# Performance work log

Hardware: AMD Instinct MI355X
Metric: run time of the kernel (lower is better)

The kernel has to match this reference:

```python
import jax, jax.numpy as jnp
import numpy as np

N_HEAD = 32
N_QUERY_GROUPS = 8
HEAD_SIZE = 128
N_EMBD = 4096


def apply_rope(x, cos, sin):
    # x: [B, H, T, D]; cos/sin: [T, D] (rotary_percentage = 1.0 so D = head_size)
    d = x.shape[-1]
    x1, x2 = x[..., : d // 2], x[..., d // 2:]
    rotated = jnp.concatenate([-x2, x1], axis=-1)
    return x * cos + rotated * sin


def setup_inputs() -> dict:
    key = jax.random.key(0)
    k1, k2, k3, k4, k5 = jax.random.split(key, 5)
    B, T = 1, 2048
    x = jax.random.normal(k1, (B, T, N_EMBD), dtype=jnp.float32)
    # realistic rope angles
    theta = 10000.0 ** (-jnp.arange(0, HEAD_SIZE // 2, dtype=jnp.float32) * 2.0 / HEAD_SIZE)
    ang = jnp.arange(T, dtype=jnp.float32)[:, None] * theta[None, :]
    ang = jnp.concatenate([ang, ang], axis=-1)  # [T, HEAD_SIZE]
    cos, sin = jnp.cos(ang), jnp.sin(ang)
    qkv_dim = (N_HEAD + 2 * N_QUERY_GROUPS) * HEAD_SIZE  # 6144
    w_attn = jax.random.normal(k2, (qkv_dim, N_EMBD), dtype=jnp.float32) * (N_EMBD ** -0.5)
    w_proj = jax.random.normal(k3, (N_EMBD, N_HEAD * HEAD_SIZE), dtype=jnp.float32) * ((N_HEAD * HEAD_SIZE) ** -0.5)
    return {"x": x, "cos": cos, "sin": sin, "w_attn": w_attn, "w_proj": w_proj}


def reference(x, cos, sin, w_attn, w_proj):
    B, T, C = x.shape
    G, hs = N_QUERY_GROUPS, HEAD_SIZE
    q_per_kv = N_HEAD // G  # 4
    total_qkv = q_per_kv + 2

    qkv = jnp.einsum('btc,oc->bto', x, w_attn)  # [B, T, 6144]
    qkv = qkv.reshape(B, T, G, total_qkv, hs).transpose(0, 2, 3, 1, 4)  # [B, G, total, T, hs]
    q = qkv[:, :, :q_per_kv]              # [B, G, qpk, T, hs]
    k = qkv[:, :, q_per_kv:q_per_kv + 1]  # [B, G, 1,   T, hs]
    v = qkv[:, :, q_per_kv + 1:]          # [B, G, 1,   T, hs]

    # GQA expand to per-query heads, then flatten head dims
    k = jnp.broadcast_to(k, (B, G, q_per_kv, T, hs))
    v = jnp.broadcast_to(v, (B, G, q_per_kv, T, hs))
    q = q.reshape(B, N_HEAD, T, hs)
    k = k.reshape(B, N_HEAD, T, hs)
    v = v.reshape(B, N_HEAD, T, hs)

    # rotary_percentage = 1.0 -> rope over full head dim
    q = apply_rope(q, cos, sin)
    k = apply_rope(k, cos, sin)

    scale = 1.0 / jnp.sqrt(jnp.float32(hs))
    scores = jnp.einsum('bhqd,bhkd->bhqk', q, k) * scale  # [B, H, T, T]
    causal = jnp.tril(jnp.ones((T, T), dtype=bool))
    scores = jnp.where(causal, scores, jnp.finfo(scores.dtype).min)
    attn = jax.nn.softmax(scores, axis=-1)
    y = jnp.einsum('bhqk,bhkd->bhqd', attn, v)  # [B, H, T, hs]
    y = y.transpose(0, 2, 1, 3).reshape(B, T, N_HEAD * hs)
    return jnp.einsum('bto,co->btc', y, w_proj)  # [B, T, C]
```

## Files before the change

kernel.cpp:

```cpp
#include <hip/hip_runtime.h>
#include <hip/hip_bf16.h>

typedef __attribute__((ext_vector_type(8))) short short8;
typedef __attribute__((ext_vector_type(4))) float f32x4;

__device__ inline unsigned short f2bf(float f) {
  __hip_bfloat16 h = __float2bfloat16(f);
  return *reinterpret_cast<unsigned short*>(&h);
}
__device__ inline float bf2f(unsigned short u) {
  union { unsigned u; float f; } v; v.u = ((unsigned)u) << 16;
  return v.f;
}

#define GLOAD_LDS16(g, l)                                          \
  __builtin_amdgcn_global_load_lds(                                \
      (const __attribute__((address_space(1))) void*)(g),          \
      (__attribute__((address_space(3))) void*)(l), 16, 0, 0)

__global__ void f32_to_bf16(const float* __restrict__ in,
                            unsigned short* __restrict__ out, int n8) {
  int i = blockIdx.x * 256 + threadIdx.x;
  if (i >= n8) return;
  const float4* p = (const float4*)in + (size_t)i * 2;
  float4 a = p[0], b = p[1];
  short8 v;
  v[0] = f2bf(a.x); v[1] = f2bf(a.y); v[2] = f2bf(a.z); v[3] = f2bf(a.w);
  v[4] = f2bf(b.x); v[5] = f2bf(b.y); v[6] = f2bf(b.z); v[7] = f2bf(b.w);
  *((short8*)out + i) = v;
}

template <bool OUT_F32>
__global__ __launch_bounds__(256, 3)
void gemm_bt_bf16(const unsigned short* __restrict__ A,
                  const unsigned short* __restrict__ B,
                  void* __restrict__ Cp, int M, int N, int K) {
  __shared__ __align__(16) unsigned short As[128 * 32];
  __shared__ __align__(16) unsigned short Bs[128 * 32];
  const int t = threadIdx.x;
  const int lane = t & 63, w = t >> 6;
  const int wr = w >> 1, wc = w & 1;
  const int r16 = lane & 15, kg = lane >> 4;
  const int bm = blockIdx.x, bn = blockIdx.y;

  const int srow = w * 16 + (lane >> 2);
  const int scol = (lane & 3) * 8;

  const unsigned short* Ag = A + (size_t)(bm * 128) * K;
  const unsigned short* Bg = B + (size_t)(bn * 128) * K;

  f32x4 acc[4][4] = {};

  for (int k0 = 0; k0 < K; k0 += 32) {
    __syncthreads();
#pragma unroll
    for (int i = 0; i < 2; ++i) {
      GLOAD_LDS16(Ag + (size_t)(i * 64 + srow) * K + k0 + scol,
                  As + i * 2048 + w * 512);
      GLOAD_LDS16(Bg + (size_t)(i * 64 + srow) * K + k0 + scol,
                  Bs + i * 2048 + w * 512);
    }
    __syncthreads();

    short8 a[4], b[4];
#pragma unroll
    for (int m = 0; m < 4; ++m)
      a[m] = *(const short8*)&As[(wr * 64 + m * 16 + r16) * 32 + kg * 8];
#pragma unroll
    for (int n = 0; n < 4; ++n)
      b[n] = *(const short8*)&Bs[(wc * 64 + n * 16 + r16) * 32 + kg * 8];
#pragma unroll
    for (int m = 0; m < 4; ++m)
#pragma unroll
      for (int n = 0; n < 4; ++n)
        acc[m][n] = __builtin_amdgcn_mfma_f32_16x16x32_bf16(a[m], b[n], acc[m][n], 0, 0, 0);
  }

#pragma unroll
  for (int m = 0; m < 4; ++m) {
#pragma unroll
    for (int n = 0; n < 4; ++n) {
#pragma unroll
      for (int j = 0; j < 4; ++j) {
        int row = bm * 128 + wr * 64 + m * 16 + kg * 4 + j;
        int col = bn * 128 + wc * 64 + n * 16 + r16;
        if (OUT_F32) ((float*)Cp)[(size_t)row * N + col] = acc[m][n][j];
        else ((unsigned short*)Cp)[(size_t)row * N + col] = f2bf(acc[m][n][j]);
      }
    }
  }
}

__global__ void rope_qk(const unsigned short* __restrict__ qkv,
                        const float* __restrict__ cosb, const float* __restrict__ sinb,
                        unsigned short* __restrict__ Q, unsigned short* __restrict__ K) {
  int pair = blockIdx.x * 4 + (threadIdx.x >> 6);
  int l = threadIdx.x & 63;
  int t = pair / 40, slot = pair - t * 40;
  const unsigned short* src;
  unsigned short* dst;
  float scale;
  if (slot < 32) {
    int g = slot >> 2, j = slot & 3;
    src = qkv + (size_t)t * 6144 + g * 768 + j * 128;
    dst = Q + ((size_t)slot * 2048 + t) * 128;
    scale = 0.08838834764831845f;
  } else {
    int g = slot - 32;
    src = qkv + (size_t)t * 6144 + g * 768 + 512;
    dst = K + ((size_t)g * 2048 + t) * 128;
    scale = 1.0f;
  }
  float x1 = bf2f(src[l]), x2 = bf2f(src[64 + l]);
  float c1 = cosb[t * 128 + l], s1 = sinb[t * 128 + l];
  float c2 = cosb[t * 128 + 64 + l], s2 = sinb[t * 128 + 64 + l];
  dst[l]      = f2bf((x1 * c1 - x2 * s1) * scale);
  dst[64 + l] = f2bf((x2 * c2 + x1 * s2) * scale);
}

__global__ void transpose_v(const unsigned short* __restrict__ qkv,
                            unsigned short* __restrict__ Vt) {
  __shared__ __align__(16) unsigned short tile[64][136];
  int g = blockIdx.y, t0 = blockIdx.x * 64;
  int th = threadIdx.x;
  int r = th >> 2, c0 = (th & 3) * 32;
  const unsigned short* src = qkv + (size_t)(t0 + r) * 6144 + g * 768 + 640 + c0;
#pragma unroll
  for (int i = 0; i < 4; ++i)
    *(short8*)&tile[r][c0 + i * 8] = *(const short8*)(src + i * 8);
  __syncthreads();
  int d = th >> 1, tc = (th & 1) * 32;
  unsigned short* dst = Vt + (size_t)(g * 128 + d) * 2048 + t0 + tc;
#pragma unroll
  for (int j = 0; j < 32; ++j) dst[j] = tile[tc + j][d];
}

__global__ __launch_bounds__(256, 2)
void flash_attn(const unsigned short* __restrict__ Q, const unsigned short* __restrict__ K,
                const unsigned short* __restrict__ Vt, unsigned short* __restrict__ Y) {
  __shared__ __align__(16) unsigned short Ksm[2][64 * 128];
  __shared__ __align__(16) unsigned short Vsm[2][128 * 64];

  const int h = blockIdx.y, g = h >> 2;
  const int t = threadIdx.x, lane = t & 63, w = t >> 6;
  const int r16 = lane & 15, kg = lane >> 4;
  const bool odd = kg & 1;
  const bool hi = kg >> 1;
  const bool useswap = odd ^ hi;

  const unsigned short* Kg = K + (size_t)g * 2048 * 128;
  const unsigned short* Vg = Vt + (size_t)g * 128 * 2048;

  const int krl = lane >> 4, kc = lane & 15;
  const int vrl = lane >> 3, vc = lane & 7;

  auto stage = [&](int kvs, int b) {
#pragma unroll
    for (int i = 0; i < 4; ++i) {
      int row = w * 16 + i * 4 + krl;
      int sc = kc ^ (row & 7);
      GLOAD_LDS16(Kg + (size_t)(kvs + row) * 128 + sc * 8,
                  &Ksm[b][(w * 16 + i * 4) * 128]);
    }
#pragma unroll
    for (int i = 0; i < 4; ++i) {
      int d = w * 32 + i * 8 + vrl;
      int sc = vc ^ (d & 7);
      GLOAD_LDS16(Vg + (size_t)d * 2048 + kvs + sc * 8,
                  &Vsm[b][(w * 32 + i * 8) * 64]);
    }
  };

  auto process = [&](int q0) {
    short8 qf[4];
    const unsigned short* qrow = Q + ((size_t)h * 2048 + q0 + w * 16 + r16) * 128;
#pragma unroll
    for (int kk = 0; kk < 4; ++kk) qf[kk] = *(const short8*)(qrow + kk * 32 + kg * 8);

    f32x4 o[8] = {};
    float mrow = -1e30f, lrow = 0.f;
    const int qg = q0 + w * 16 + r16;
    const int nt = q0 / 64 + 1;

    __syncthreads();
    stage(0, 0);

    for (int kt = 0; kt < nt; ++kt) {
      const int b = kt & 1;
      const int kv0 = kt * 64;
      __syncthreads();
      if (kt + 1 < nt) stage((kt + 1) * 64, b ^ 1);

      f32x4 s[4] = {};
      __builtin_amdgcn_s_setprio(1);
#pragma unroll
      for (int n = 0; n < 4; ++n) {
        int kr = n * 16 + r16;
#pragma unroll
        for (int kk = 0; kk < 4; ++kk) {
          short8 kf = *(const short8*)__builtin_assume_aligned(
              &Ksm[b][kr * 128 + ((kk * 32 + kg * 8) ^ ((kr & 7) << 3))], 16);
          s[n] = __builtin_amdgcn_mfma_f32_16x16x32_bf16(kf, qf[kk], s[n], 0, 0, 0);
        }
      }
      __builtin_amdgcn_s_setprio(0);

      if (kv0 + 63 > q0 + w * 16) {
#pragma unroll
        for (int n = 0; n < 4; ++n)
#pragma unroll
          for (int j = 0; j < 4; ++j)
            if (kv0 + n * 16 + kg * 4 + j > qg) s[n][j] = -1e30f;
      }

      float rmax = -1e30f;
#pragma unroll
      for (int n = 0; n < 4; ++n)
#pragma unroll
        for (int j = 0; j < 4; ++j) rmax = fmaxf(rmax, s[n][j]);
      rmax = fmaxf(rmax, __shfl_xor(rmax, 16));
      rmax = fmaxf(rmax, __shfl_xor(rmax, 32));

      if (__builtin_amdgcn_ballot_w64(rmax > mrow)) {
        float mnew = fmaxf(mrow, rmax);
        float fac = __expf(mrow - mnew);
        mrow = mnew;
        lrow *= fac;
        float fj[4];
#pragma unroll
        for (int j = 0; j < 4; ++j) fj[j] = __shfl(fac, kg * 4 + j);
#pragma unroll
        for (int f = 0; f < 8; ++f)
#pragma unroll
          for (int j = 0; j < 4; ++j) o[f][j] *= fj[j];
      }

      float p[4][4];
      float rs = 0.f;
#pragma unroll
      for (int n = 0; n < 4; ++n)
#pragma unroll
        for (int j = 0; j < 4; ++j) {
          p[n][j] = __expf(s[n][j] - mrow);
          rs += p[n][j];
        }
      rs += __shfl_xor(rs, 16);
      rs += __shfl_xor(rs, 32);
      lrow += rs;

      unsigned bpk[4][2], xpk[4][2];
#pragma unroll
      for (int n = 0; n < 4; ++n)
#pragma unroll
        for (int i = 0; i < 2; ++i)
          bpk[n][i] = (unsigned)f2bf(p[n][2 * i]) | ((unsigned)f2bf(p[n][2 * i + 1]) << 16);
#pragma unroll
      for (int n = 0; n < 4; ++n)
#pragma unroll
        for (int i = 0; i < 2; ++i) xpk[n][i] = __shfl_xor(bpk[n][i], 16);

      unsigned pl[4][2], ph[4][2];
#pragma unroll
      for (int n = 0; n < 4; ++n)
#pragma unroll
        for (int i = 0; i < 2; ++i) {
          pl[n][i] = odd ? xpk[n][i] : bpk[n][i];
          ph[n][i] = odd ? bpk[n][i] : xpk[n][i];
        }

      short8 pa[2];
#pragma unroll
      for (int kk = 0; kk < 2; ++kk) {
        unsigned kp0 = hi ? pl[2 * kk + 1][0] : pl[2 * kk][0];
        unsigned kp1 = hi ? pl[2 * kk + 1][1] : pl[2 * kk][1];
        unsigned kp2 = hi ? ph[2 * kk + 1][0] : ph[2 * kk][0];
        unsigned kp3 = hi ? ph[2 * kk + 1][1] : ph[2 * kk][1];
        unsigned sd0 = hi ? pl[2 * kk][0] : pl[2 * kk + 1][0];
        unsigned sd1 = hi ? pl[2 * kk][1] : pl[2 * kk + 1][1];
        unsigned sd2 = hi ? ph[2 * kk][0] : ph[2 * kk + 1][0];
        unsigned sd3 = hi ? ph[2 * kk][1] : ph[2 * kk + 1][1];
        unsigned g0 = __shfl_xor(sd0, 32), g1 = __shfl_xor(sd1, 32);
        unsigned g2 = __shfl_xor(sd2, 32), g3 = __shfl_xor(sd3, 32);
        union { unsigned u[4]; short8 v; } pu;
        pu.u[0] = useswap ? g0 : kp0;
        pu.u[1] = useswap ? g1 : kp1;
        pu.u[2] = useswap ? g2 : kp2;
        pu.u[3] = useswap ? g3 : kp3;
        pa[kk] = pu.v;
      }

      __builtin_amdgcn_s_setprio(1);
#pragma unroll
      for (int kk = 0; kk < 2; ++kk) {
#pragma unroll
        for (int f = 0; f < 8; ++f) {
          int d = f * 16 + r16;
          short8 vf = *(const short8*)__builtin_assume_aligned(
              &Vsm[b][d * 64 + ((kk * 32 + kg * 8) ^ ((d & 7) << 3))], 16);
          o[f] = __builtin_amdgcn_mfma_f32_16x16x32_bf16(pa[kk], vf, o[f], 0, 0, 0);
        }
      }
      __builtin_amdgcn_s_setprio(0);
    }

    float inv = 1.f / lrow;
    float invj[4];
#pragma unroll
    for (int j = 0; j < 4; ++j) invj[j] = __shfl(inv, kg * 4 + j);
#pragma unroll
    for (int j = 0; j < 4; ++j) {
      int row = q0 + w * 16 + kg * 4 + j;
      unsigned short* yr = Y + (size_t)row * 4096 + h * 128;
#pragma unroll
      for (int f = 0; f < 8; ++f) yr[f * 16 + r16] = f2bf(o[f][j] * invj[j]);
    }
  };

  const int pr = blockIdx.x;
  process(pr * 64);
  process((31 - pr) * 64);
}

extern "C" void kernel_launch(void* const* d_in, const int* in_sizes, int n_in,
                              void* d_out, int out_size, void* d_ws, size_t ws_size,
                              hipStream_t stream) {
  const float* x      = (const float*)d_in[0];
  const float* cosb   = (const float*)d_in[1];
  const float* sinb   = (const float*)d_in[2];
  const float* w_attn = (const float*)d_in[3];
  const float* w_proj = (const float*)d_in[4];
  float* out = (float*)d_out;

  char* ws = (char*)d_ws;
  const size_t MB = 1024 * 1024;
  unsigned short* Xb  = (unsigned short*)(ws);
  unsigned short* Wa  = (unsigned short*)(ws + 16 * MB);
  unsigned short* Wp  = (unsigned short*)(ws);
  unsigned short* Qb  = (unsigned short*)(ws + 32 * MB);
  unsigned short* Kb  = (unsigned short*)(ws + 48 * MB);
  unsigned short* Vt  = (unsigned short*)(ws + 52 * MB);
  unsigned short* qkv = (unsigned short*)(ws + 64 * MB);
  unsigned short* Yb  = (unsigned short*)(ws + 64 * MB);

  f32_to_bf16<<<4096, 256, 0, stream>>>(x, Xb, 2048 * 4096 / 8);
  f32_to_bf16<<<12288, 256, 0, stream>>>(w_attn, Wa, 6144 * 4096 / 8);
  gemm_bt_bf16<false><<<dim3(16, 48), 256, 0, stream>>>(Xb, Wa, qkv, 2048, 6144, 4096);
  rope_qk<<<20480, 256, 0, stream>>>(qkv, cosb, sinb, Qb, Kb);
  transpose_v<<<dim3(32, 8), 256, 0, stream>>>(qkv, Vt);
  f32_to_bf16<<<8192, 256, 0, stream>>>(w_proj, Wp, 4096 * 4096 / 8);
  flash_attn<<<dim3(16, 32), 256, 0, stream>>>(Qb, Kb, Vt, Yb);
  gemm_bt_bf16<true><<<dim3(16, 32), 256, 0, stream>>>(Yb, Wp, out, 2048, 4096, 4096);
}
```

Measured before the change: 351.6 us.

## Replace GEMM with 256-row tiled, double-buffered, swizzled LDS pipeline

Replaces the 128x128, single-buffered bf16 GEMM with a 512-thread kernel using 256xBN tiles, a K-step of 64, double-buffered LDS with async global-to-LDS prefetch two steps ahead, XOR-swizzled LDS layout, and interleaved MFMA phases with priority hints. It targets the per-step sync stalls, low data reuse and LDS bank conflicts of the old GEMM, for both the QKV and output projections. In exchange it uses much more LDS and registers, launches fewer blocks (192 and 256), and relies on fragile hand-placed waitcnt and barriers.

```diff
diff --git a/kernel.cpp b/kernel.cpp
--- a/kernel.cpp
+++ b/kernel.cpp
@@ -30,60 +30,142 @@
   *((short8*)out + i) = v;
 }
 
-template <bool OUT_F32>
-__global__ __launch_bounds__(256, 3)
-void gemm_bt_bf16(const unsigned short* __restrict__ A,
-                  const unsigned short* __restrict__ B,
-                  void* __restrict__ Cp, int M, int N, int K) {
-  __shared__ __align__(16) unsigned short As[128 * 32];
-  __shared__ __align__(16) unsigned short Bs[128 * 32];
-  const int t = threadIdx.x;
-  const int lane = t & 63, w = t >> 6;
-  const int wr = w >> 1, wc = w & 1;
+template <int BN, bool OUT_F32>
+__global__ __launch_bounds__(512, 2)
+void gemm256(const unsigned short* __restrict__ A, const unsigned short* __restrict__ B,
+             void* __restrict__ Cp, int M, int N, int K, int nbm) {
+  constexpr int BPARTS = BN / 128;
+  constexpr int WN = BN / 4;
+  constexpr int NREP = WN / 16;
+  constexpr int NQ = NREP / 2;
+  constexpr int LPK = 4 + 2 * BPARTS;
+
+  __shared__ __align__(16) unsigned short lds[2][2 + BPARTS][128 * 64];
+
+  const int t = threadIdx.x, lane = t & 63, w = t >> 6;
+  const int wm = w >> 2, wn = w & 3;
   const int r16 = lane & 15, kg = lane >> 4;
-  const int bm = blockIdx.x, bn = blockIdx.y;
-
-  const int srow = w * 16 + (lane >> 2);
-  const int scol = (lane & 3) * 8;
-
-  const unsigned short* Ag = A + (size_t)(bm * 128) * K;
-  const unsigned short* Bg = B + (size_t)(bn * 128) * K;
-
-  f32x4 acc[4][4] = {};
-
-  for (int k0 = 0; k0 < K; k0 += 32) {
-    __syncthreads();
+  const int bid = blockIdx.x;
+  const int bm = bid % nbm, bn = bid / nbm;
+  const int NT = K >> 6;
+
+  const int sr = lane >> 3, sch = lane & 7;
+  const unsigned short* Ag = A + (size_t)(bm * 256) * K;
+  const unsigned short* Bg = B + (size_t)(bn * BN) * K;
+
+  auto stageA = [&](int kt, int h, int b) {
 #pragma unroll
     for (int i = 0; i < 2; ++i) {
-      GLOAD_LDS16(Ag + (size_t)(i * 64 + srow) * K + k0 + scol,
-                  As + i * 2048 + w * 512);
-      GLOAD_LDS16(Bg + (size_t)(i * 64 + srow) * K + k0 + scol,
-                  Bs + i * 2048 + w * 512);
-    }
-    __syncthreads();
-
-    short8 a[4], b[4];
-#pragma unroll
-    for (int m = 0; m < 4; ++m)
-      a[m] = *(const short8*)&As[(wr * 64 + m * 16 + r16) * 32 + kg * 8];
-#pragma unroll
-    for (int n = 0; n < 4; ++n)
-      b[n] = *(const short8*)&Bs[(wc * 64 + n * 16 + r16) * 32 + kg * 8];
-#pragma unroll
-    for (int m = 0; m < 4; ++m)
-#pragma unroll
-      for (int n = 0; n < 4; ++n)
-        acc[m][n] = __builtin_amdgcn_mfma_f32_16x16x32_bf16(a[m], b[n], acc[m][n], 0, 0, 0);
+      int rb = w * 16 + i * 8;
+      int rl = rb + sr;
+      int sc = sch ^ (rl & 7);
+      GLOAD_LDS16(Ag + (size_t)(h * 128 + rl) * K + kt * 64 + sc * 8,
+                  &lds[b][h][rb * 64]);
+    }
+  };
+  auto stageB = [&](int kt, int h, int b) {
+#pragma unroll
+    for (int i = 0; i < 2; ++i) {
+      int rb = w * 16 + i * 8;
+      int rl = rb + sr;
+      int sc = sch ^ (rl & 7);
+      GLOAD_LDS16(Bg + (size_t)(h * 128 + rl) * K + kt * 64 + sc * 8,
+                  &lds[b][2 + h][rb * 64]);
+    }
+  };
+
+  const int bpart = (wn * WN) >> 7;
+  const int brow0 = (wn * WN) & 127;
+
+  auto lda = [&](int b, int m, int kk) -> short8 {
+    int rp = m * 16 + r16;
+    int ch = (kk * 4 + kg) ^ (rp & 7);
+    return *(const short8*)__builtin_assume_aligned(&lds[b][wm][rp * 64 + ch * 8], 16);
+  };
+  auto ldb = [&](int b, int n, int kk) -> short8 {
+    int rp = brow0 + n * 16 + r16;
+    int ch = (kk * 4 + kg) ^ (rp & 7);
+    return *(const short8*)__builtin_assume_aligned(&lds[b][2 + bpart][rp * 64 + ch * 8], 16);
+  };
+
+  f32x4 acc[8][NREP] = {};
+  short8 a0[4][2], a1[4][2], bb[NREP][2];
+
+#define MFMA_Q(AARR, MB, NB)                                                   \
+  _Pragma("unroll") for (int m = 0; m < 4; ++m)                                \
+  _Pragma("unroll") for (int n = 0; n < NQ; ++n)                               \
+  _Pragma("unroll") for (int kk = 0; kk < 2; ++kk)                             \
+      acc[MB + m][NB + n] = __builtin_amdgcn_mfma_f32_16x16x32_bf16(           \
+          AARR[m][kk], bb[NB + n][kk], acc[MB + m][NB + n], 0, 0, 0);
+
+#define LGKM0_FENCE()                                       \
+  asm volatile("s_waitcnt lgkmcnt(0)" ::: "memory");        \
+  __builtin_amdgcn_sched_barrier(0);
+
+  stageB(0, 0, 0); if (BPARTS == 2) stageB(0, 1, 0);
+  stageA(0, 0, 0); stageA(0, 1, 0);
+  stageB(1, 0, 1); if (BPARTS == 2) stageB(1, 1, 1);
+  stageA(1, 0, 1); stageA(1, 1, 1);
+  asm volatile("s_waitcnt vmcnt(%0)" :: "n"(LPK) : "memory");
+  __builtin_amdgcn_s_barrier();
+
+  for (int kt = 0; kt < NT; ++kt) {
+    const int b = kt & 1;
+    const bool pf = (kt + 2) < NT;
+
+#pragma unroll
+    for (int m = 0; m < 4; ++m) { a0[m][0] = lda(b, m, 0); a0[m][1] = lda(b, m, 1); }
+#pragma unroll
+    for (int n = 0; n < NQ; ++n) { bb[n][0] = ldb(b, n, 0); bb[n][1] = ldb(b, n, 1); }
+    __builtin_amdgcn_s_barrier();
+    LGKM0_FENCE();
+    __builtin_amdgcn_s_setprio(1);
+    MFMA_Q(a0, 0, 0);
+    __builtin_amdgcn_s_setprio(0);
+    __builtin_amdgcn_s_barrier();
+
+#pragma unroll
+    for (int n = 0; n < NQ; ++n) { bb[NQ + n][0] = ldb(b, NQ + n, 0); bb[NQ + n][1] = ldb(b, NQ + n, 1); }
+    __builtin_amdgcn_s_barrier();
+    LGKM0_FENCE();
+    __builtin_amdgcn_s_setprio(1);
+    MFMA_Q(a0, 0, NQ);
+    __builtin_amdgcn_s_setprio(0);
+    __builtin_amdgcn_s_barrier();
+
+#pragma unroll
+    for (int m = 0; m < 4; ++m) { a1[m][0] = lda(b, 4 + m, 0); a1[m][1] = lda(b, 4 + m, 1); }
+    if (pf) { stageB(kt + 2, 0, b); if (BPARTS == 2) stageB(kt + 2, 1, b); }
+    __builtin_amdgcn_s_barrier();
+    LGKM0_FENCE();
+    __builtin_amdgcn_s_setprio(1);
+    MFMA_Q(a1, 4, NQ);
+    __builtin_amdgcn_s_setprio(0);
+    __builtin_amdgcn_s_barrier();
+
+    if (pf) { stageA(kt + 2, 0, b); stageA(kt + 2, 1, b); }
+    __builtin_amdgcn_s_barrier();
+    __builtin_amdgcn_s_setprio(1);
+    MFMA_Q(a1, 4, 0);
+    __builtin_amdgcn_s_setprio(0);
+    if (kt + 1 < NT) {
+      if (pf) asm volatile("s_waitcnt vmcnt(%0)" :: "n"(LPK) : "memory");
+      else    asm volatile("s_waitcnt vmcnt(0)" ::: "memory");
+      __builtin_amdgcn_sched_barrier(0);
+      __builtin_amdgcn_s_barrier();
+    }
   }
-
-#pragma unroll
-  for (int m = 0; m < 4; ++m) {
-#pragma unroll
-    for (int n = 0; n < 4; ++n) {
+#undef MFMA_Q
+#undef LGKM0_FENCE
+
+#pragma unroll
+  for (int m = 0; m < 8; ++m) {
+#pragma unroll
+    for (int n = 0; n < NREP; ++n) {
 #pragma unroll
       for (int j = 0; j < 4; ++j) {
-        int row = bm * 128 + wr * 64 + m * 16 + kg * 4 + j;
-        int col = bn * 128 + wc * 64 + n * 16 + r16;
+        int row = bm * 256 + wm * 128 + m * 16 + kg * 4 + j;
+        int col = bn * BN + wn * WN + n * 16 + r16;
         if (OUT_F32) ((float*)Cp)[(size_t)row * N + col] = acc[m][n][j];
         else ((unsigned short*)Cp)[(size_t)row * N + col] = f2bf(acc[m][n][j]);
       }
@@ -344,10 +426,10 @@
 
   f32_to_bf16<<<4096, 256, 0, stream>>>(x, Xb, 2048 * 4096 / 8);
   f32_to_bf16<<<12288, 256, 0, stream>>>(w_attn, Wa, 6144 * 4096 / 8);
-  gemm_bt_bf16<false><<<dim3(16, 48), 256, 0, stream>>>(Xb, Wa, qkv, 2048, 6144, 4096);
+  gemm256<256, false><<<192, 512, 0, stream>>>(Xb, Wa, qkv, 2048, 6144, 4096, 8);
   rope_qk<<<20480, 256, 0, stream>>>(qkv, cosb, sinb, Qb, Kb);
   transpose_v<<<dim3(32, 8), 256, 0, stream>>>(qkv, Vt);
   f32_to_bf16<<<8192, 256, 0, stream>>>(w_proj, Wp, 4096 * 4096 / 8);
   flash_attn<<<dim3(16, 32), 256, 0, stream>>>(Qb, Kb, Vt, Yb);
-  gemm_bt_bf16<true><<<dim3(16, 32), 256, 0, stream>>>(Yb, Wp, out, 2048, 4096, 4096);
-}
+  gemm256<128, true><<<256, 512, 0, stream>>>(Yb, Wp, out, 2048, 4096, 4096, 8);
+}
```

After: 341.2 us. -3.0%, faster.

## Replace generic GEMM with pipelined, swizzled, larger-tile QKV and projection GEMMs

Applied to the files above, without the earlier changes.

Replaces the simple single-buffered 128x128x32 GEMM with two specialised 512-thread kernels. They use 256x192 and 128x256 tiles, K-step 64, double-buffered LDS filled by direct global-to-LDS loads, and an XOR swizzle to avoid LDS bank conflicts. Prefetch of later k-tiles is interleaved with MFMA phases, using explicit vmcnt waits, barriers and setprio so that memory traffic overlaps compute. Each launch is 256 blocks, one wave of work on the 256 CUs. The cost is much more hand-scheduled code and larger LDS and register use per block.

```diff
diff --git a/kernel.cpp b/kernel.cpp
--- a/kernel.cpp
+++ b/kernel.cpp
@@ -17,6 +17,12 @@
   __builtin_amdgcn_global_load_lds(                                \
       (const __attribute__((address_space(1))) void*)(g),          \
       (__attribute__((address_space(3))) void*)(l), 16, 0, 0)
+
+#define MFMA16(a, b, c) __builtin_amdgcn_mfma_f32_16x16x32_bf16((a), (b), (c), 0, 0, 0)
+
+#define LGKM0()                                              \
+  asm volatile("s_waitcnt lgkmcnt(0)" ::: "memory");         \
+  __builtin_amdgcn_sched_barrier(0);
 
 __global__ void f32_to_bf16(const float* __restrict__ in,
                             unsigned short* __restrict__ out, int n8) {
@@ -30,65 +36,215 @@
   *((short8*)out + i) = v;
 }
 
-template <bool OUT_F32>
-__global__ __launch_bounds__(256, 3)
-void gemm_bt_bf16(const unsigned short* __restrict__ A,
-                  const unsigned short* __restrict__ B,
-                  void* __restrict__ Cp, int M, int N, int K) {
-  __shared__ __align__(16) unsigned short As[128 * 32];
-  __shared__ __align__(16) unsigned short Bs[128 * 32];
-  const int t = threadIdx.x;
-  const int lane = t & 63, w = t >> 6;
-  const int wr = w >> 1, wc = w & 1;
+__global__ __launch_bounds__(512, 2)
+void gemm_qkv(const unsigned short* __restrict__ A, const unsigned short* __restrict__ B,
+              unsigned short* __restrict__ C, int M, int N, int K) {
+  __shared__ __align__(16) unsigned short lds[2][448 * 64];
+  const int t = threadIdx.x, lane = t & 63, w = t >> 6;
+  const int wm = w >> 2, wn = w & 3;
   const int r16 = lane & 15, kg = lane >> 4;
-  const int bm = blockIdx.x, bn = blockIdx.y;
-
-  const int srow = w * 16 + (lane >> 2);
-  const int scol = (lane & 3) * 8;
-
-  const unsigned short* Ag = A + (size_t)(bm * 128) * K;
-  const unsigned short* Bg = B + (size_t)(bn * 128) * K;
-
-  f32x4 acc[4][4] = {};
-
-  for (int k0 = 0; k0 < K; k0 += 32) {
-    __syncthreads();
-#pragma unroll
-    for (int i = 0; i < 2; ++i) {
-      GLOAD_LDS16(Ag + (size_t)(i * 64 + srow) * K + k0 + scol,
-                  As + i * 2048 + w * 512);
-      GLOAD_LDS16(Bg + (size_t)(i * 64 + srow) * K + k0 + scol,
-                  Bs + i * 2048 + w * 512);
-    }
-    __syncthreads();
-
-    short8 a[4], b[4];
+  const int bm = blockIdx.x & 7, bn = blockIdx.x >> 3;
+  const int NT = K >> 6;
+  const int sr = lane >> 3, sch = lane & 7;
+  const unsigned short* Ag = A + (size_t)(bm * 256) * K;
+  const unsigned short* Bg = B + (size_t)(bn * 192) * K;
+
+  auto stA = [&](int kt, int j, int b) {
+    int rl = j * 64 + w * 8 + sr, sc = sch ^ (rl & 7);
+    GLOAD_LDS16(Ag + (size_t)rl * K + kt * 64 + sc * 8, &lds[b][(j * 64 + w * 8) * 64]);
+  };
+  auto stB = [&](int kt, int j, int b) {
+    int rl = j * 64 + w * 8 + sr, sc = sch ^ (rl & 7);
+    GLOAD_LDS16(Bg + (size_t)rl * K + kt * 64 + sc * 8, &lds[b][(256 + j * 64 + w * 8) * 64]);
+  };
+  auto lda = [&](int b, int m, int kk) -> short8 {
+    int row = wm * 128 + m * 16 + r16, ch = (kk * 4 + kg) ^ (row & 7);
+    return *(const short8*)__builtin_assume_aligned(&lds[b][row * 64 + ch * 8], 16);
+  };
+  auto ldb = [&](int b, int n, int kk) -> short8 {
+    int row = wn * 48 + n * 16 + r16, ch = (kk * 4 + kg) ^ (row & 7);
+    return *(const short8*)__builtin_assume_aligned(&lds[b][(256 + row) * 64 + ch * 8], 16);
+  };
+
+  f32x4 acc[8][3] = {};
+  short8 a0[4][2], a1[4][2], bb[3][2];
+
+#pragma unroll
+  for (int j = 0; j < 4; ++j) stA(0, j, 0);
+#pragma unroll
+  for (int j = 0; j < 3; ++j) stB(0, j, 0);
+#pragma unroll
+  for (int j = 0; j < 3; ++j) stA(1, j, 1);
+#pragma unroll
+  for (int j = 0; j < 3; ++j) stB(1, j, 1);
+  asm volatile("s_waitcnt vmcnt(6)" ::: "memory");
+  __builtin_amdgcn_sched_barrier(0);
+  __builtin_amdgcn_s_barrier();
+
+  for (int kt = 0; kt < NT; ++kt) {
+    const int b = kt & 1;
+    const bool pf1 = kt + 1 < NT, pf2 = kt + 2 < NT;
+
+    if (pf1) stA(kt + 1, 3, b ^ 1);
+#pragma unroll
+    for (int m = 0; m < 4; ++m) { a0[m][0] = lda(b, m, 0); a0[m][1] = lda(b, m, 1); }
+#pragma unroll
+    for (int n = 0; n < 2; ++n) { bb[n][0] = ldb(b, n, 0); bb[n][1] = ldb(b, n, 1); }
+    __builtin_amdgcn_s_barrier();
+    LGKM0();
+    __builtin_amdgcn_s_setprio(1);
 #pragma unroll
     for (int m = 0; m < 4; ++m)
-      a[m] = *(const short8*)&As[(wr * 64 + m * 16 + r16) * 32 + kg * 8];
-#pragma unroll
-    for (int n = 0; n < 4; ++n)
-      b[n] = *(const short8*)&Bs[(wc * 64 + n * 16 + r16) * 32 + kg * 8];
+#pragma unroll
+      for (int n = 0; n < 2; ++n)
+#pragma unroll
+        for (int kk = 0; kk < 2; ++kk) acc[m][n] = MFMA16(a0[m][kk], bb[n][kk], acc[m][n]);
+    __builtin_amdgcn_s_setprio(0);
+    __builtin_amdgcn_s_barrier();
+
+    bb[2][0] = ldb(b, 2, 0); bb[2][1] = ldb(b, 2, 1);
+#pragma unroll
+    for (int m = 0; m < 4; ++m) { a1[m][0] = lda(b, 4 + m, 0); a1[m][1] = lda(b, 4 + m, 1); }
+    if (pf2) { stA(kt + 2, 0, b); stA(kt + 2, 2, b); }
+    __builtin_amdgcn_s_barrier();
+    LGKM0();
+    __builtin_amdgcn_s_setprio(1);
 #pragma unroll
     for (int m = 0; m < 4; ++m)
 #pragma unroll
-      for (int n = 0; n < 4; ++n)
-        acc[m][n] = __builtin_amdgcn_mfma_f32_16x16x32_bf16(a[m], b[n], acc[m][n], 0, 0, 0);
-  }
-
-#pragma unroll
-  for (int m = 0; m < 4; ++m) {
-#pragma unroll
-    for (int n = 0; n < 4; ++n) {
-#pragma unroll
-      for (int j = 0; j < 4; ++j) {
-        int row = bm * 128 + wr * 64 + m * 16 + kg * 4 + j;
-        int col = bn * 128 + wc * 64 + n * 16 + r16;
-        if (OUT_F32) ((float*)Cp)[(size_t)row * N + col] = acc[m][n][j];
-        else ((unsigned short*)Cp)[(size_t)row * N + col] = f2bf(acc[m][n][j]);
-      }
+      for (int kk = 0; kk < 2; ++kk) acc[m][2] = MFMA16(a0[m][kk], bb[2][kk], acc[m][2]);
+#pragma unroll
+    for (int m = 0; m < 4; ++m)
+#pragma unroll
+      for (int kk = 0; kk < 2; ++kk) acc[4 + m][2] = MFMA16(a1[m][kk], bb[2][kk], acc[4 + m][2]);
+    __builtin_amdgcn_s_setprio(0);
+    __builtin_amdgcn_s_barrier();
+
+    if (pf2) { stB(kt + 2, 0, b); stB(kt + 2, 1, b); stB(kt + 2, 2, b); stA(kt + 2, 1, b); }
+    __builtin_amdgcn_s_barrier();
+    __builtin_amdgcn_s_setprio(1);
+#pragma unroll
+    for (int m = 0; m < 4; ++m)
+#pragma unroll
+      for (int n = 0; n < 2; ++n)
+#pragma unroll
+        for (int kk = 0; kk < 2; ++kk) acc[4 + m][n] = MFMA16(a1[m][kk], bb[n][kk], acc[4 + m][n]);
+    __builtin_amdgcn_s_setprio(0);
+    if (pf1) {
+      if (pf2) asm volatile("s_waitcnt vmcnt(6)" ::: "memory");
+      else     asm volatile("s_waitcnt vmcnt(0)" ::: "memory");
+      __builtin_amdgcn_sched_barrier(0);
+      __builtin_amdgcn_s_barrier();
     }
   }
+
+#pragma unroll
+  for (int m = 0; m < 8; ++m)
+#pragma unroll
+    for (int n = 0; n < 3; ++n)
+#pragma unroll
+      for (int j = 0; j < 4; ++j) {
+        int row = bm * 256 + wm * 128 + m * 16 + kg * 4 + j;
+        int col = bn * 192 + wn * 48 + n * 16 + r16;
+        C[(size_t)row * N + col] = f2bf(acc[m][n][j]);
+      }
+}
+
+__global__ __launch_bounds__(512, 2)
+void gemm_proj(const unsigned short* __restrict__ A, const unsigned short* __restrict__ B,
+               float* __restrict__ C, int M, int N, int K) {
+  __shared__ __align__(16) unsigned short lds[2][384 * 64];
+  const int t = threadIdx.x, lane = t & 63, w = t >> 6;
+  const int wm = w >> 2, wn = w & 3;
+  const int r16 = lane & 15, kg = lane >> 4;
+  const int bm = blockIdx.x & 15, bn = blockIdx.x >> 4;
+  const int NT = K >> 6;
+  const int sr = lane >> 3, sch = lane & 7;
+  const unsigned short* Ag = A + (size_t)(bm * 128) * K;
+  const unsigned short* Bg = B + (size_t)(bn * 256) * K;
+
+  auto stA = [&](int kt, int j, int b) {
+    int rl = j * 64 + w * 8 + sr, sc = sch ^ (rl & 7);
+    GLOAD_LDS16(Ag + (size_t)rl * K + kt * 64 + sc * 8, &lds[b][(j * 64 + w * 8) * 64]);
+  };
+  auto stB = [&](int kt, int j, int b) {
+    int rl = j * 64 + w * 8 + sr, sc = sch ^ (rl & 7);
+    GLOAD_LDS16(Bg + (size_t)rl * K + kt * 64 + sc * 8, &lds[b][(128 + j * 64 + w * 8) * 64]);
+  };
+  auto lda = [&](int b, int m, int kk) -> short8 {
+    int row = wm * 64 + m * 16 + r16, ch = (kk * 4 + kg) ^ (row & 7);
+    return *(const short8*)__builtin_assume_aligned(&lds[b][row * 64 + ch * 8], 16);
+  };
+  auto ldb = [&](int b, int n, int kk) -> short8 {
+    int row = wn * 64 + n * 16 + r16, ch = (kk * 4 + kg) ^ (row & 7);
+    return *(const short8*)__builtin_assume_aligned(&lds[b][(128 + row) * 64 + ch * 8], 16);
+  };
+
+  f32x4 acc[4][4] = {};
+  short8 af[4][2], bb[4][2];
+
+#pragma unroll
+  for (int j = 0; j < 2; ++j) stA(0, j, 0);
+#pragma unroll
+  for (int j = 0; j < 4; ++j) stB(0, j, 0);
+#pragma unroll
+  for (int j = 0; j < 2; ++j) stA(1, j, 1);
+  asm volatile("s_waitcnt vmcnt(2)" ::: "memory");
+  __builtin_amdgcn_sched_barrier(0);
+  __builtin_amdgcn_s_barrier();
+
+  for (int kt = 0; kt < NT; ++kt) {
+    const int b = kt & 1;
+    const bool pf1 = kt + 1 < NT, pf2 = kt + 2 < NT;
+
+    if (pf1) { stB(kt + 1, 0, b ^ 1); stB(kt + 1, 1, b ^ 1); stB(kt + 1, 2, b ^ 1); stB(kt + 1, 3, b ^ 1); }
+#pragma unroll
+    for (int m = 0; m < 4; ++m) { af[m][0] = lda(b, m, 0); af[m][1] = lda(b, m, 1); }
+#pragma unroll
+    for (int n = 0; n < 2; ++n) { bb[n][0] = ldb(b, n, 0); bb[n][1] = ldb(b, n, 1); }
+    __builtin_amdgcn_s_barrier();
+    LGKM0();
+    __builtin_amdgcn_s_setprio(1);
+#pragma unroll
+    for (int m = 0; m < 4; ++m)
+#pragma unroll
+      for (int n = 0; n < 2; ++n)
+#pragma unroll
+        for (int kk = 0; kk < 2; ++kk) acc[m][n] = MFMA16(af[m][kk], bb[n][kk], acc[m][n]);
+    __builtin_amdgcn_s_setprio(0);
+    __builtin_amdgcn_s_barrier();
+
+#pragma unroll
+    for (int n = 2; n < 4; ++n) { bb[n][0] = ldb(b, n, 0); bb[n][1] = ldb(b, n, 1); }
+    if (pf2) { stA(kt + 2, 0, b); stA(kt + 2, 1, b); }
+    __builtin_amdgcn_s_barrier();
+    LGKM0();
+    __builtin_amdgcn_s_setprio(1);
+#pragma unroll
+    for (int m = 0; m < 4; ++m)
+#pragma unroll
+      for (int n = 2; n < 4; ++n)
+#pragma unroll
+        for (int kk = 0; kk < 2; ++kk) acc[m][n] = MFMA16(af[m][kk], bb[n][kk], acc[m][n]);
+    __builtin_amdgcn_s_setprio(0);
+    if (pf1) {
+      if (pf2) asm volatile("s_waitcnt vmcnt(2)" ::: "memory");
+      else     asm volatile("s_waitcnt vmcnt(0)" ::: "memory");
+      __builtin_amdgcn_sched_barrier(0);
+      __builtin_amdgcn_s_barrier();
+    }
+  }
+
+#pragma unroll
+  for (int m = 0; m < 4; ++m)
+#pragma unroll
+    for (int n = 0; n < 4; ++n)
+#pragma unroll
+      for (int j = 0; j < 4; ++j) {
+        int row = bm * 128 + wm * 64 + m * 16 + kg * 4 + j;
+        int col = bn * 256 + wn * 64 + n * 16 + r16;
+        C[(size_t)row * N + col] = acc[m][n][j];
+      }
 }
 
 __global__ void rope_qk(const unsigned short* __restrict__ qkv,
@@ -344,10 +500,10 @@
 
   f32_to_bf16<<<4096, 256, 0, stream>>>(x, Xb, 2048 * 4096 / 8);
   f32_to_bf16<<<12288, 256, 0, stream>>>(w_attn, Wa, 6144 * 4096 / 8);
-  gemm_bt_bf16<false><<<dim3(16, 48), 256, 0, stream>>>(Xb, Wa, qkv, 2048, 6144, 4096);
+  gemm_qkv<<<256, 512, 0, stream>>>(Xb, Wa, qkv, 2048, 6144, 4096);
   rope_qk<<<20480, 256, 0, stream>>>(qkv, cosb, sinb, Qb, Kb);
   transpose_v<<<dim3(32, 8), 256, 0, stream>>>(qkv, Vt);
   f32_to_bf16<<<8192, 256, 0, stream>>>(w_proj, Wp, 4096 * 4096 / 8);
   flash_attn<<<dim3(16, 32), 256, 0, stream>>>(Qb, Kb, Vt, Yb);
-  gemm_bt_bf16<true><<<dim3(16, 32), 256, 0, stream>>>(Yb, Wp, out, 2048, 4096, 4096);
-}
+  gemm_proj<<<256, 512, 0, stream>>>(Yb, Wp, out, 2048, 4096, 4096);
+}
```

Measured after the change: 315.5 us. -10.3%, faster.
